# Optimization experiments

Hardware: AMD Instinct MI355X
Metric: run time of the kernel (lower is better)

Reference implementation:

```python
import jax, jax.numpy as jnp
import numpy as np
from jax import lax

VOCAB, EMBED_DIM, NUM_TAGS = 50000, 300, 16
BATCH, SEQ = 64, 512


def setup_inputs() -> dict:
    key = jax.random.key(0)
    k0, k1, k2, k3, k4 = jax.random.split(key, 5)
    text = jax.random.randint(k0, (BATCH, SEQ), 0, VOCAB)
    tags = jax.random.randint(k1, (BATCH, SEQ), 0, NUM_TAGS)
    embed_table = jax.random.normal(k2, (VOCAB, EMBED_DIM), jnp.float32) * 0.02
    W = jax.random.normal(k3, (EMBED_DIM, NUM_TAGS), jnp.float32) * 0.05
    b = jnp.zeros((NUM_TAGS,), jnp.float32)
    trans = jax.random.uniform(k4, (NUM_TAGS, NUM_TAGS), jnp.float32)
    return {"text": text, "tags": tags, "embed_table": embed_table, "W": W, "b": b, "trans": trans}


def crf_log_likelihood(probs, tags, lens, trans):
    # probs: [B,S,T] unary potentials; tags: [B,S] int; lens: [B]; trans: [T,T]
    B, S, T = probs.shape
    t_idx = jnp.arange(S)
    mask = (t_idx[None, :] < lens[:, None])  # [B,S] valid positions

    # --- gold sequence score ---
    unary = jnp.take_along_axis(probs, tags[..., None], axis=2)[..., 0]  # [B,S]
    unary_score = jnp.sum(unary * mask, axis=1)
    btrans = trans[tags[:, :-1], tags[:, 1:]]            # [B,S-1]
    bmask = mask[:, 1:]                                   # transition t->t+1 valid iff t+1 < len
    binary_score = jnp.sum(btrans * bmask, axis=1)

    # --- forward algorithm (log partition) ---
    alpha0 = probs[:, 0]                                  # [B,T]
    emits = jnp.moveaxis(probs[:, 1:], 0, 1)              # [S-1,B,T]
    ms = jnp.moveaxis(mask[:, 1:], 0, 1)                  # [S-1,B]

    def step(alpha, inp):
        emit, m = inp
        new = jax.nn.logsumexp(alpha[:, :, None] + trans[None, :, :], axis=1) + emit
        return jnp.where(m[:, None], new, alpha), None

    alpha, _ = lax.scan(step, alpha0, (emits, ms))
    log_norm = jax.nn.logsumexp(alpha, axis=-1)           # [B]
    return unary_score + binary_score - log_norm


def reference(text, tags, embed_table, W, b, trans):
    # dropout is identity in eval/reference mode
    text_lens = jnp.sum((text != 0).astype(jnp.int32), axis=1)  # [B]
    probs = embed_table[text] @ W + b                            # [B,S,T]
    log_likelihood = crf_log_likelihood(probs, tags, text_lens, trans)
    return probs, text_lens, log_likelihood
```

## Files before the change

kernel.cpp:

```cpp
#include <hip/hip_runtime.h>
#include <hip/hip_bf16.h>

#define VOCAB 50000
#define ED    300
#define NT    16
#define BB    64
#define SS    512

#define LOG2E 1.4426950408889634f
#define LN2   0.6931471805599453f

#define WSTR 308

__global__ __launch_bounds__(256) void probs_kernel(const int* __restrict__ text,
                                                    const float* __restrict__ emb,
                                                    const float* __restrict__ W,
                                                    const float* __restrict__ bias,
                                                    float* __restrict__ out_probs) {
  __shared__ float wt[NT * WSTR];

  const int tid = threadIdx.x;
  const int lane = tid & 63, wave = tid >> 6;
  const int r = lane >> 4, t = lane & 15;
  const int row = blockIdx.x * 16 + wave * 4 + r;

  for (int e = tid; e < ED * NT; e += 256) {
    int d = e >> 4, tt = e & 15;
    wt[tt * WSTR + d] = W[e];
  }

  const int tok = text[row];
  const float4* erow = (const float4*)(emb + (size_t)tok * ED);
  float acc = bias[t];

  float4 A[8];
#pragma unroll
  for (int i = 0; i < 8; ++i) A[i] = erow[i];

  __syncthreads();

  const float4* w4 = (const float4*)(wt + t * WSTR);
#pragma unroll
  for (int c = 0; c < 75; ++c) {
    float4 e = A[c % 8];
    if (c < 67) A[c % 8] = erow[c + 8];
    float4 w = w4[c];
    acc = fmaf(e.x, w.x, acc);
    acc = fmaf(e.y, w.y, acc);
    acc = fmaf(e.z, w.z, acc);
    acc = fmaf(e.w, w.w, acc);
  }
  out_probs[(size_t)row * NT + t] = acc;
}

template <int CTRL>
__device__ __forceinline__ float dppmov(float x) {
  int xi = __float_as_int(x);
  return __int_as_float(
      __builtin_amdgcn_update_dpp(xi, xi, CTRL, 0xF, 0xF, false));
}

__device__ __forceinline__ float crf_step(float g, float pe, const float E[16]) {
  float gn, h, m, c, a1, a2, a3;
  asm("s_nop 1\n\t"
      "v_mov_b32_dpp %[h], %[g] row_half_mirror row_mask:0xf bank_mask:0xf\n\t"
      "v_mov_b32_dpp %[m], %[g] row_mirror row_mask:0xf bank_mask:0xf\n\t"
      "v_mul_f32 %[gn], %[g], %[e0]\n\t"
      "v_fmac_f32_dpp %[gn], %[g], %[e1] quad_perm:[1,0,3,2] row_mask:0xf bank_mask:0xf\n\t"
      "v_fmac_f32_dpp %[gn], %[g], %[e2] quad_perm:[2,3,0,1] row_mask:0xf bank_mask:0xf\n\t"
      "v_fmac_f32_dpp %[gn], %[g], %[e3] quad_perm:[3,2,1,0] row_mask:0xf bank_mask:0xf\n\t"
      "v_mov_b32_dpp %[c], %[m] row_half_mirror row_mask:0xf bank_mask:0xf\n\t"
      "v_mul_f32 %[a1], %[h], %[e7]\n\t"
      "v_fmac_f32_dpp %[a1], %[h], %[e6] quad_perm:[1,0,3,2] row_mask:0xf bank_mask:0xf\n\t"
      "v_fmac_f32_dpp %[a1], %[h], %[e5] quad_perm:[2,3,0,1] row_mask:0xf bank_mask:0xf\n\t"
      "v_fmac_f32_dpp %[a1], %[h], %[e4] quad_perm:[3,2,1,0] row_mask:0xf bank_mask:0xf\n\t"
      "v_mul_f32 %[a2], %[m], %[e15]\n\t"
      "v_fmac_f32_dpp %[a2], %[m], %[e14] quad_perm:[1,0,3,2] row_mask:0xf bank_mask:0xf\n\t"
      "v_fmac_f32_dpp %[a2], %[m], %[e13] quad_perm:[2,3,0,1] row_mask:0xf bank_mask:0xf\n\t"
      "v_fmac_f32_dpp %[a2], %[m], %[e12] quad_perm:[3,2,1,0] row_mask:0xf bank_mask:0xf\n\t"
      "v_mul_f32 %[a3], %[c], %[e8]\n\t"
      "v_fmac_f32_dpp %[a3], %[c], %[e9] quad_perm:[1,0,3,2] row_mask:0xf bank_mask:0xf\n\t"
      "v_fmac_f32_dpp %[a3], %[c], %[e10] quad_perm:[2,3,0,1] row_mask:0xf bank_mask:0xf\n\t"
      "v_fmac_f32_dpp %[a3], %[c], %[e11] quad_perm:[3,2,1,0] row_mask:0xf bank_mask:0xf\n\t"
      "v_add_f32 %[gn], %[gn], %[a1]\n\t"
      "v_add_f32 %[a2], %[a2], %[a3]\n\t"
      "v_add_f32 %[gn], %[gn], %[a2]\n\t"
      "v_mul_f32 %[gn], %[gn], %[pe]"
      : [gn] "=&v"(gn), [h] "=&v"(h), [m] "=&v"(m), [c] "=&v"(c),
        [a1] "=&v"(a1), [a2] "=&v"(a2), [a3] "=&v"(a3)
      : [g] "v"(g), [pe] "v"(pe),
        [e0] "v"(E[0]), [e1] "v"(E[1]), [e2] "v"(E[2]), [e3] "v"(E[3]),
        [e4] "v"(E[4]), [e5] "v"(E[5]), [e6] "v"(E[6]), [e7] "v"(E[7]),
        [e8] "v"(E[8]), [e9] "v"(E[9]), [e10] "v"(E[10]), [e11] "v"(E[11]),
        [e12] "v"(E[12]), [e13] "v"(E[13]), [e14] "v"(E[14]), [e15] "v"(E[15]));
  return gn;
}

__global__ __launch_bounds__(64) void crf_kernel(const int* __restrict__ text,
                                                 const int* __restrict__ tags,
                                                 const float* __restrict__ trans,
                                                 const float* __restrict__ probs,
                                                 float* __restrict__ out_lens,
                                                 float* __restrict__ out_ll) {
  __shared__ float lps[(SS + 1) * NT];
  __shared__ int tgs[SS];
  __shared__ float trs[256];

  const int tid = threadIdx.x;
  const int j = tid & 15;
  const int b = blockIdx.x;

  {
    const float4* p4 = (const float4*)(probs + (size_t)b * SS * NT);
    float4* l4 = (float4*)lps;
#pragma unroll
    for (int i = 0; i < 32; ++i) {
      float4 v = p4[tid + 64 * i];
      v.x *= LOG2E; v.y *= LOG2E; v.z *= LOG2E; v.w *= LOG2E;
      l4[tid + 64 * i] = v;
    }
    const int4* t4 = (const int4*)(tags + b * SS);
    int4* lt = (int4*)tgs;
#pragma unroll
    for (int i = 0; i < 2; ++i) lt[tid + 64 * i] = t4[tid + 64 * i];
    for (int i = tid; i < 256; i += 64) trs[i] = trans[i];
  }
  __syncthreads();

  const int* tx = text + b * SS;
  int cnt = 0;
#pragma unroll
  for (int k = 0; k < 8; ++k) cnt += (tx[tid + 64 * k] != 0) ? 1 : 0;
  for (int off = 32; off > 0; off >>= 1) cnt += __shfl_xor(cnt, off, 64);
  const int len = cnt;
  if (tid == 0) out_lens[b] = (float)len;

  float su = 0.f, sb = 0.f;
#pragma unroll
  for (int it = 0; it < 8; ++it) {
    const int s = tid + 64 * it;
    if (s < len) {
      int t1 = tgs[s];
      su += lps[s * NT + t1];
      if (s >= 1) sb += trs[tgs[s - 1] * 16 + t1];
    }
  }
  float sc = fmaf(su, LN2, sb);
  for (int off = 32; off > 0; off >>= 1) sc += __shfl_xor(sc, off, 64);

  float E[16];
#pragma unroll
  for (int k = 0; k < 16; ++k) E[k] = __expf(trs[((j ^ k) << 4) + j]);

  float g = exp2f(lps[j]);
  float K2 = 0.f;

  const int T = (len > 0) ? len - 1 : 0;
  const int nfull = T >> 4;
  const int rem = T & 15;

  float raw[16];
#pragma unroll
  for (int c = 0; c < 16; ++c) raw[c] = lps[(1 + c) * NT + j];

  int s0 = 1;
  for (int blk = 0; blk < nfull; ++blk) {
#pragma unroll
    for (int c = 0; c < 16; ++c) {
      float pe = exp2f(raw[c]);
      raw[c] = lps[(s0 + 16 + c) * NT + j];
      g = crf_step(g, pe, E);
    }
    float mx = g;
    mx = fmaxf(mx, dppmov<0xB1>(mx));
    mx = fmaxf(mx, dppmov<0x4E>(mx));
    mx = fmaxf(mx, dppmov<0x141>(mx));
    mx = fmaxf(mx, dppmov<0x140>(mx));
    float rr = 1.0f / mx;
    K2 -= __log2f(rr);
    g *= rr;
    s0 += 16;
  }
  for (int c = 0; c < rem; ++c) {
    float pe = exp2f(raw[c]);
    g = crf_step(g, pe, E);
  }

  float x = g;
  x += dppmov<0xB1>(x);
  x += dppmov<0x4E>(x);
  x += dppmov<0x141>(x);
  x += dppmov<0x140>(x);
  float log_norm = LN2 * (K2 + __log2f(x));
  if (tid == 0) out_ll[b] = sc - log_norm;
}

extern "C" void kernel_launch(void* const* d_in, const int* in_sizes, int n_in,
                              void* d_out, int out_size, void* d_ws, size_t ws_size,
                              hipStream_t stream) {
  const int* text = (const int*)d_in[0];
  const int* tags = (const int*)d_in[1];
  const float* emb = (const float*)d_in[2];
  const float* W = (const float*)d_in[3];
  const float* bias = (const float*)d_in[4];
  const float* trans = (const float*)d_in[5];

  float* out = (float*)d_out;
  float* out_probs = out;
  float* out_lens = out + BB * SS * NT;
  float* out_ll = out + BB * SS * NT + BB;

  probs_kernel<<<(BB * SS) / 16, 256, 0, stream>>>(text, emb, W, bias, out_probs);
  crf_kernel<<<BB, 64, 0, stream>>>(text, tags, trans, out_probs, out_lens, out_ll);
}
```

Measured before the change: 151.7 us.

## Fuse probs and CRF kernels into one cooperative kernel with grid sync

Merges the embedding-projection kernel and the CRF forward kernel into a single cooperative launch. The two stages are separated by a grid-wide barrier, and the projection work is spread over 256 blocks of 1024 threads, each thread computing two rows. The shared-memory weight tile is reused as the CRF staging buffer. This removes one kernel launch and the gap between kernels. In exchange it adds grid-sync overhead and changes the projection work split, while the CRF stage still runs on only 64 single-wave blocks.

```diff
diff --git a/kernel.cpp b/kernel.cpp
--- a/kernel.cpp
+++ b/kernel.cpp
@@ -1,5 +1,7 @@
 #include <hip/hip_runtime.h>
 #include <hip/hip_bf16.h>
+#include <hip/hip_cooperative_groups.h>
+namespace cg = cooperative_groups;
 
 #define VOCAB 50000
 #define ED    300
@@ -9,49 +11,9 @@
 
 #define LOG2E 1.4426950408889634f
 #define LN2   0.6931471805599453f
-
-#define WSTR 308
-
-__global__ __launch_bounds__(256) void probs_kernel(const int* __restrict__ text,
-                                                    const float* __restrict__ emb,
-                                                    const float* __restrict__ W,
-                                                    const float* __restrict__ bias,
-                                                    float* __restrict__ out_probs) {
-  __shared__ float wt[NT * WSTR];
-
-  const int tid = threadIdx.x;
-  const int lane = tid & 63, wave = tid >> 6;
-  const int r = lane >> 4, t = lane & 15;
-  const int row = blockIdx.x * 16 + wave * 4 + r;
-
-  for (int e = tid; e < ED * NT; e += 256) {
-    int d = e >> 4, tt = e & 15;
-    wt[tt * WSTR + d] = W[e];
-  }
-
-  const int tok = text[row];
-  const float4* erow = (const float4*)(emb + (size_t)tok * ED);
-  float acc = bias[t];
-
-  float4 A[8];
-#pragma unroll
-  for (int i = 0; i < 8; ++i) A[i] = erow[i];
-
-  __syncthreads();
-
-  const float4* w4 = (const float4*)(wt + t * WSTR);
-#pragma unroll
-  for (int c = 0; c < 75; ++c) {
-    float4 e = A[c % 8];
-    if (c < 67) A[c % 8] = erow[c + 8];
-    float4 w = w4[c];
-    acc = fmaf(e.x, w.x, acc);
-    acc = fmaf(e.y, w.y, acc);
-    acc = fmaf(e.z, w.z, acc);
-    acc = fmaf(e.w, w.w, acc);
-  }
-  out_probs[(size_t)row * NT + t] = acc;
-}
+#define WSTR  308
+#define GRID  256
+#define BLK   1024
 
 template <int CTRL>
 __device__ __forceinline__ float dppmov(float x) {
@@ -96,49 +58,87 @@
   return gn;
 }
 
-__global__ __launch_bounds__(64) void crf_kernel(const int* __restrict__ text,
-                                                 const int* __restrict__ tags,
-                                                 const float* __restrict__ trans,
-                                                 const float* __restrict__ probs,
-                                                 float* __restrict__ out_lens,
-                                                 float* __restrict__ out_ll) {
-  __shared__ float lps[(SS + 1) * NT];
-  __shared__ int tgs[SS];
-  __shared__ float trs[256];
+__global__ __launch_bounds__(BLK, 4) void fused_kernel(
+    const int* __restrict__ text, const int* __restrict__ tags,
+    const float* __restrict__ emb, const float* __restrict__ W,
+    const float* __restrict__ bias, const float* __restrict__ trans,
+    float* __restrict__ out_probs, float* __restrict__ out_lens,
+    float* __restrict__ out_ll) {
+  __shared__ float smem[8976];
+  float* wt = smem;
+  float* lps = smem;
+  int* tgs = (int*)(smem + 8208);
+  float* trs = smem + 8208 + 512;
 
   const int tid = threadIdx.x;
-  const int j = tid & 15;
+  const int wave = tid >> 6, lane = tid & 63;
+  const int r = lane >> 4, t = lane & 15;
+
+  for (int e = tid; e < ED * NT; e += BLK) {
+    int d = e >> 4, tt = e & 15;
+    wt[tt * WSTR + d] = W[e];
+  }
+
+  const int row0 = blockIdx.x * 128 + wave * 8 + r;
+  const int tok0 = text[row0];
+  const int tok1 = text[row0 + 4];
+  const float4* er0 = (const float4*)(emb + (size_t)tok0 * ED);
+  const float4* er1 = (const float4*)(emb + (size_t)tok1 * ED);
+  float acc0 = bias[t];
+  float acc1 = acc0;
+
+  float4 A0[4], A1[4];
+#pragma unroll
+  for (int i = 0; i < 4; ++i) { A0[i] = er0[i]; A1[i] = er1[i]; }
+
+  __syncthreads();
+
+  const float4* w4 = (const float4*)(wt + t * WSTR);
+#pragma unroll
+  for (int c = 0; c < 75; ++c) {
+    float4 e0 = A0[c & 3], e1 = A1[c & 3];
+    if (c < 71) { A0[c & 3] = er0[c + 4]; A1[c & 3] = er1[c + 4]; }
+    float4 w = w4[c];
+    acc0 = fmaf(e0.x, w.x, acc0); acc0 = fmaf(e0.y, w.y, acc0);
+    acc0 = fmaf(e0.z, w.z, acc0); acc0 = fmaf(e0.w, w.w, acc0);
+    acc1 = fmaf(e1.x, w.x, acc1); acc1 = fmaf(e1.y, w.y, acc1);
+    acc1 = fmaf(e1.z, w.z, acc1); acc1 = fmaf(e1.w, w.w, acc1);
+  }
+  out_probs[(size_t)row0 * NT + t] = acc0;
+  out_probs[(size_t)(row0 + 4) * NT + t] = acc1;
+
+  cg::this_grid().sync();
+
   const int b = blockIdx.x;
+  if (b >= BB) return;
 
   {
-    const float4* p4 = (const float4*)(probs + (size_t)b * SS * NT);
+    const float4* p4 = (const float4*)(out_probs + (size_t)b * SS * NT);
     float4* l4 = (float4*)lps;
 #pragma unroll
-    for (int i = 0; i < 32; ++i) {
-      float4 v = p4[tid + 64 * i];
+    for (int i = 0; i < 2; ++i) {
+      float4 v = p4[tid + BLK * i];
       v.x *= LOG2E; v.y *= LOG2E; v.z *= LOG2E; v.w *= LOG2E;
-      l4[tid + 64 * i] = v;
+      l4[tid + BLK * i] = v;
     }
-    const int4* t4 = (const int4*)(tags + b * SS);
-    int4* lt = (int4*)tgs;
-#pragma unroll
-    for (int i = 0; i < 2; ++i) lt[tid + 64 * i] = t4[tid + 64 * i];
-    for (int i = tid; i < 256; i += 64) trs[i] = trans[i];
+    if (tid < 128) ((int4*)tgs)[tid] = ((const int4*)(tags + b * SS))[tid];
+    if (tid < 256) trs[tid] = trans[tid];
   }
   __syncthreads();
+  if (wave != 0) return;
 
   const int* tx = text + b * SS;
   int cnt = 0;
 #pragma unroll
-  for (int k = 0; k < 8; ++k) cnt += (tx[tid + 64 * k] != 0) ? 1 : 0;
+  for (int k = 0; k < 8; ++k) cnt += (tx[lane + 64 * k] != 0) ? 1 : 0;
   for (int off = 32; off > 0; off >>= 1) cnt += __shfl_xor(cnt, off, 64);
   const int len = cnt;
-  if (tid == 0) out_lens[b] = (float)len;
+  if (lane == 0) out_lens[b] = (float)len;
 
   float su = 0.f, sb = 0.f;
 #pragma unroll
   for (int it = 0; it < 8; ++it) {
-    const int s = tid + 64 * it;
+    const int s = lane + 64 * it;
     if (s < len) {
       int t1 = tgs[s];
       su += lps[s * NT + t1];
@@ -148,6 +148,7 @@
   float sc = fmaf(su, LN2, sb);
   for (int off = 32; off > 0; off >>= 1) sc += __shfl_xor(sc, off, 64);
 
+  const int j = lane & 15;
   float E[16];
 #pragma unroll
   for (int k = 0; k < 16; ++k) E[k] = __expf(trs[((j ^ k) << 4) + j]);
@@ -192,7 +193,7 @@
   x += dppmov<0x141>(x);
   x += dppmov<0x140>(x);
   float log_norm = LN2 * (K2 + __log2f(x));
-  if (tid == 0) out_ll[b] = sc - log_norm;
+  if (lane == 0) out_ll[b] = sc - log_norm;
 }
 
 extern "C" void kernel_launch(void* const* d_in, const int* in_sizes, int n_in,
@@ -210,6 +211,9 @@
   float* out_lens = out + BB * SS * NT;
   float* out_ll = out + BB * SS * NT + BB;
 
-  probs_kernel<<<(BB * SS) / 16, 256, 0, stream>>>(text, emb, W, bias, out_probs);
-  crf_kernel<<<BB, 64, 0, stream>>>(text, tags, trans, out_probs, out_lens, out_ll);
-}
+  void* args[] = {(void*)&text, (void*)&tags, (void*)&emb,   (void*)&W,
+                  (void*)&bias, (void*)&trans, (void*)&out_probs,
+                  (void*)&out_lens, (void*)&out_ll};
+  hipLaunchCooperativeKernel((void*)fused_kernel, dim3(GRID), dim3(BLK), args,
+                             0, stream);
+}
```

Measured after the change: 194.7 us. 1.28x slower.

## Fuse probs and CRF kernels with per-batch atomic completion flags

Applied to the files above, without the earlier changes.

Merges the projection kernel and the CRF forward kernel into one launch. Each block bumps a per-batch counter after writing its probs, and the first block of each batch spins until all 32 sibling blocks finish, then runs the CRF recursion reading probs straight from global/L2 instead of staging them in LDS. This removes the dependency between two kernels and lets CRF work for finished batches overlap with projection of others. It adds a tiny flag-init kernel, relies on the producer blocks of a batch being scheduled while the waiter spins, and puts global-load latency on the serial recursion path.

```diff
diff --git a/kernel.cpp b/kernel.cpp
--- a/kernel.cpp
+++ b/kernel.cpp
@@ -9,48 +9,10 @@
 
 #define LOG2E 1.4426950408889634f
 #define LN2   0.6931471805599453f
-
-#define WSTR 308
-
-__global__ __launch_bounds__(256) void probs_kernel(const int* __restrict__ text,
-                                                    const float* __restrict__ emb,
-                                                    const float* __restrict__ W,
-                                                    const float* __restrict__ bias,
-                                                    float* __restrict__ out_probs) {
-  __shared__ float wt[NT * WSTR];
-
-  const int tid = threadIdx.x;
-  const int lane = tid & 63, wave = tid >> 6;
-  const int r = lane >> 4, t = lane & 15;
-  const int row = blockIdx.x * 16 + wave * 4 + r;
-
-  for (int e = tid; e < ED * NT; e += 256) {
-    int d = e >> 4, tt = e & 15;
-    wt[tt * WSTR + d] = W[e];
-  }
-
-  const int tok = text[row];
-  const float4* erow = (const float4*)(emb + (size_t)tok * ED);
-  float acc = bias[t];
-
-  float4 A[8];
-#pragma unroll
-  for (int i = 0; i < 8; ++i) A[i] = erow[i];
-
-  __syncthreads();
-
-  const float4* w4 = (const float4*)(wt + t * WSTR);
-#pragma unroll
-  for (int c = 0; c < 75; ++c) {
-    float4 e = A[c % 8];
-    if (c < 67) A[c % 8] = erow[c + 8];
-    float4 w = w4[c];
-    acc = fmaf(e.x, w.x, acc);
-    acc = fmaf(e.y, w.y, acc);
-    acc = fmaf(e.z, w.z, acc);
-    acc = fmaf(e.w, w.w, acc);
-  }
-  out_probs[(size_t)row * NT + t] = acc;
+#define WSTR  308
+
+__global__ __launch_bounds__(64) void init_flags(unsigned int* __restrict__ f) {
+  f[threadIdx.x] = 0u;
 }
 
 template <int CTRL>
@@ -96,63 +58,92 @@
   return gn;
 }
 
-__global__ __launch_bounds__(64) void crf_kernel(const int* __restrict__ text,
-                                                 const int* __restrict__ tags,
-                                                 const float* __restrict__ trans,
-                                                 const float* __restrict__ probs,
-                                                 float* __restrict__ out_lens,
-                                                 float* __restrict__ out_ll) {
-  __shared__ float lps[(SS + 1) * NT];
-  __shared__ int tgs[SS];
-  __shared__ float trs[256];
+__global__ __launch_bounds__(256, 6) void main_kernel(
+    const int* __restrict__ text, const int* __restrict__ tags,
+    const float* __restrict__ emb, const float* __restrict__ W,
+    const float* __restrict__ bias, const float* __restrict__ trans,
+    float* __restrict__ out_probs, float* __restrict__ out_lens,
+    float* __restrict__ out_ll, unsigned int* __restrict__ flags) {
+  __shared__ float wt[NT * WSTR];
 
   const int tid = threadIdx.x;
-  const int j = tid & 15;
-  const int b = blockIdx.x;
-
-  {
-    const float4* p4 = (const float4*)(probs + (size_t)b * SS * NT);
-    float4* l4 = (float4*)lps;
-#pragma unroll
-    for (int i = 0; i < 32; ++i) {
-      float4 v = p4[tid + 64 * i];
-      v.x *= LOG2E; v.y *= LOG2E; v.z *= LOG2E; v.w *= LOG2E;
-      l4[tid + 64 * i] = v;
-    }
-    const int4* t4 = (const int4*)(tags + b * SS);
-    int4* lt = (int4*)tgs;
-#pragma unroll
-    for (int i = 0; i < 2; ++i) lt[tid + 64 * i] = t4[tid + 64 * i];
-    for (int i = tid; i < 256; i += 64) trs[i] = trans[i];
-  }
+  const int lane = tid & 63, wave = tid >> 6;
+  const int r = lane >> 4, t = lane & 15;
+  const int row = blockIdx.x * 16 + wave * 4 + r;
+  const int b = blockIdx.x >> 5;
+
+  for (int e = tid; e < ED * NT; e += 256) {
+    int d = e >> 4, tt = e & 15;
+    wt[tt * WSTR + d] = W[e];
+  }
+
+  const int tok = text[row];
+  const float4* erow = (const float4*)(emb + (size_t)tok * ED);
+  float acc = bias[t];
+
+  float4 A[8];
+#pragma unroll
+  for (int i = 0; i < 8; ++i) A[i] = erow[i];
+
   __syncthreads();
 
+  const float4* w4 = (const float4*)(wt + t * WSTR);
+#pragma unroll
+  for (int c = 0; c < 75; ++c) {
+    float4 e = A[c & 7];
+    if (c < 67) A[c & 7] = erow[c + 8];
+    float4 w = w4[c];
+    acc = fmaf(e.x, w.x, acc);
+    acc = fmaf(e.y, w.y, acc);
+    acc = fmaf(e.z, w.z, acc);
+    acc = fmaf(e.w, w.w, acc);
+  }
+  out_probs[(size_t)row * NT + t] = acc;
+
+  __syncthreads();
+  if (tid == 0) {
+    __threadfence();
+    __hip_atomic_fetch_add(&flags[b], 1u, __ATOMIC_RELEASE,
+                           __HIP_MEMORY_SCOPE_AGENT);
+  }
+
+  if ((blockIdx.x & 31) != 0 || wave != 0) return;
+
+  while (__hip_atomic_load(&flags[b], __ATOMIC_ACQUIRE,
+                           __HIP_MEMORY_SCOPE_AGENT) != 32u)
+    __builtin_amdgcn_s_sleep(2);
+  __threadfence();
+
+  const float* pb = out_probs + (size_t)b * SS * NT;
+  const int* tg = tags + b * SS;
   const int* tx = text + b * SS;
+
   int cnt = 0;
 #pragma unroll
-  for (int k = 0; k < 8; ++k) cnt += (tx[tid + 64 * k] != 0) ? 1 : 0;
+  for (int k = 0; k < 8; ++k) cnt += (tx[lane + 64 * k] != 0) ? 1 : 0;
   for (int off = 32; off > 0; off >>= 1) cnt += __shfl_xor(cnt, off, 64);
   const int len = cnt;
-  if (tid == 0) out_lens[b] = (float)len;
-
-  float su = 0.f, sb = 0.f;
+  if (lane == 0) out_lens[b] = (float)len;
+
+  float su = 0.f, sbin = 0.f;
 #pragma unroll
   for (int it = 0; it < 8; ++it) {
-    const int s = tid + 64 * it;
+    const int s = lane + 64 * it;
     if (s < len) {
-      int t1 = tgs[s];
-      su += lps[s * NT + t1];
-      if (s >= 1) sb += trs[tgs[s - 1] * 16 + t1];
+      int t1 = tg[s];
+      su += pb[s * NT + t1];
+      if (s >= 1) sbin += trans[tg[s - 1] * 16 + t1];
     }
   }
-  float sc = fmaf(su, LN2, sb);
+  float sc = su + sbin;
   for (int off = 32; off > 0; off >>= 1) sc += __shfl_xor(sc, off, 64);
 
+  const int j = lane & 15;
   float E[16];
 #pragma unroll
-  for (int k = 0; k < 16; ++k) E[k] = __expf(trs[((j ^ k) << 4) + j]);
-
-  float g = exp2f(lps[j]);
+  for (int k = 0; k < 16; ++k) E[k] = __expf(trans[((j ^ k) << 4) + j]);
+
+  float g = exp2f(pb[j] * LOG2E);
   float K2 = 0.f;
 
   const int T = (len > 0) ? len - 1 : 0;
@@ -161,14 +152,14 @@
 
   float raw[16];
 #pragma unroll
-  for (int c = 0; c < 16; ++c) raw[c] = lps[(1 + c) * NT + j];
+  for (int c = 0; c < 16; ++c) raw[c] = pb[(1 + c) * NT + j];
 
   int s0 = 1;
   for (int blk = 0; blk < nfull; ++blk) {
 #pragma unroll
     for (int c = 0; c < 16; ++c) {
-      float pe = exp2f(raw[c]);
-      raw[c] = lps[(s0 + 16 + c) * NT + j];
+      float pe = exp2f(raw[c] * LOG2E);
+      raw[c] = pb[(s0 + 16 + c) * NT + j];
       g = crf_step(g, pe, E);
     }
     float mx = g;
@@ -182,7 +173,7 @@
     s0 += 16;
   }
   for (int c = 0; c < rem; ++c) {
-    float pe = exp2f(raw[c]);
+    float pe = exp2f(raw[c] * LOG2E);
     g = crf_step(g, pe, E);
   }
 
@@ -192,7 +183,7 @@
   x += dppmov<0x141>(x);
   x += dppmov<0x140>(x);
   float log_norm = LN2 * (K2 + __log2f(x));
-  if (tid == 0) out_ll[b] = sc - log_norm;
+  if (lane == 0) out_ll[b] = sc - log_norm;
 }
 
 extern "C" void kernel_launch(void* const* d_in, const int* in_sizes, int n_in,
@@ -209,7 +200,9 @@
   float* out_probs = out;
   float* out_lens = out + BB * SS * NT;
   float* out_ll = out + BB * SS * NT + BB;
-
-  probs_kernel<<<(BB * SS) / 16, 256, 0, stream>>>(text, emb, W, bias, out_probs);
-  crf_kernel<<<BB, 64, 0, stream>>>(text, tags, trans, out_probs, out_lens, out_ll);
-}
+  unsigned int* flags = (unsigned int*)d_ws;
+
+  init_flags<<<1, 64, 0, stream>>>(flags);
+  main_kernel<<<(BB * SS) / 16, 256, 0, stream>>>(
+      text, tags, emb, W, bias, trans, out_probs, out_lens, out_ll, flags);
+}
```

Result: slower. 305.6 us (+101.5%).
